# Optimization experiments

Measured on AMD Instinct MI355X. Metric: run time of the kernel, lower is better.

Reference implementation:

```python
import jax, jax.numpy as jnp
import numpy as np

B, S, D = 2, 2048, 1024
H, DK, DV = 16, 64, 64
DF = 4096
EPS = 1e-5


def _layer_norm(x, g, b):
    mu = jnp.mean(x, axis=-1, keepdims=True)
    var = jnp.mean((x - mu) ** 2, axis=-1, keepdims=True)
    return (x - mu) * jax.lax.rsqrt(var + EPS) * g + b


def setup_inputs() -> dict:
    key = jax.random.key(0)
    ks = jax.random.split(key, 12)
    s = lambda fan_in: 1.0 / np.sqrt(fan_in)
    return {
        "enc_input": jax.random.normal(ks[0], (B, S, D), dtype=jnp.float32),
        "wq": jax.random.uniform(ks[1], (D, H * DK), jnp.float32, -s(D), s(D)),
        "wk": jax.random.uniform(ks[2], (D, H * DK), jnp.float32, -s(D), s(D)),
        "wv": jax.random.uniform(ks[3], (D, H * DV), jnp.float32, -s(D), s(D)),
        "wo": jax.random.uniform(ks[4], (H * DV, D), jnp.float32, -s(H * DV), s(H * DV)),
        "w1": jax.random.uniform(ks[5], (D, DF), jnp.float32, -s(D), s(D)),
        "b1": jax.random.uniform(ks[6], (DF,), jnp.float32, -s(D), s(D)),
        "w2": jax.random.uniform(ks[7], (DF, D), jnp.float32, -s(DF), s(DF)),
        "b2": jax.random.uniform(ks[8], (D,), jnp.float32, -s(DF), s(DF)),
        "ln1_g": jnp.ones((D,), jnp.float32),
        "ln1_b": jnp.zeros((D,), jnp.float32),
        "ln2_g": jnp.ones((D,), jnp.float32),
        "ln2_b": jnp.zeros((D,), jnp.float32),
    }


def reference(enc_input, wq, wk, wv, wo, w1, b1, w2, b2, ln1_g, ln1_b, ln2_g, ln2_b):
    x = enc_input
    # QKV projections -> [B, H, S, d]
    q = (x @ wq).reshape(B, S, H, DK).transpose(0, 2, 1, 3)
    k = (x @ wk).reshape(B, S, H, DK).transpose(0, 2, 1, 3)
    v = (x @ wv).reshape(B, S, H, DV).transpose(0, 2, 1, 3)
    # scaled dot-product attention (scale = 1/sqrt(d_k), dropout is identity at eval)
    score = jnp.einsum("bhqd,bhkd->bhqk", q, k) / jnp.sqrt(jnp.float32(DK))
    attn = jax.nn.softmax(score, axis=-1)
    ctx = jnp.einsum("bhqk,bhkd->bhqd", attn, v)
    ctx = ctx.transpose(0, 2, 1, 3).reshape(B, S, H * DV)
    atn_out = ctx @ wo
    # Add & Norm 1
    h = _layer_norm(x + atn_out, ln1_g, ln1_b)
    # FFN
    ffn = jax.nn.relu(h @ w1 + b1) @ w2 + b2
    # Add & Norm 2
    return _layer_norm(h + ffn, ln2_g, ln2_b)
```

## Files before the change

kernel.cpp:

```cpp
#include <hip/hip_runtime.h>
#include <hip/hip_bf16.h>

typedef __bf16 bf16;
typedef __bf16 bf16x4 __attribute__((ext_vector_type(4)));
typedef __bf16 bf16x8 __attribute__((ext_vector_type(8)));
typedef float  f32x4  __attribute__((ext_vector_type(4)));

#define KB 2
#define KS 2048
#define KD 1024
#define KH 16
#define KM (KB*KS)
#define KQKVN 3072
#define KDF 4096

__device__ __forceinline__ f32x4 mfma16(bf16x8 a, bf16x8 b, f32x4 c) {
  return __builtin_amdgcn_mfma_f32_16x16x32_bf16(a, b, c, 0, 0, 0);
}

__device__ __forceinline__ float exp2_hw(float x) {
  float r;
  asm("v_exp_f32 %0, %1" : "=v"(r) : "v"(x));
  return r;
}

__device__ __forceinline__ void g2l16(const bf16* g, bf16* l) {
  __builtin_amdgcn_global_load_lds(
      (const __attribute__((address_space(1))) unsigned int*)g,
      (__attribute__((address_space(3))) unsigned int*)l, 16, 0, 0);
}

__global__ __launch_bounds__(256) void cvt_bf16_kernel(const float* __restrict__ in,
                                                       bf16* __restrict__ out, int n) {
  int i = (blockIdx.x * 256 + threadIdx.x) * 4;
  if (i >= n) return;
  f32x4 v = *reinterpret_cast<const f32x4*>(in + i);
  bf16x4 o;
  o[0] = (bf16)v[0]; o[1] = (bf16)v[1]; o[2] = (bf16)v[2]; o[3] = (bf16)v[3];
  *reinterpret_cast<bf16x4*>(out + i) = o;
}

struct WT4 { const float* src[4]; bf16* dst[4]; };

__global__ __launch_bounds__(256) void wtrans4_kernel(WT4 jobs) {
  __shared__ float tile[32][33];
  const float* W = jobs.src[blockIdx.z];
  bf16* WT = jobs.dst[blockIdx.z];
  const int n0 = blockIdx.x * 32, k0 = blockIdx.y * 32;
  const int tx = threadIdx.x & 31, ty = threadIdx.x >> 5;
#pragma unroll
  for (int j = ty; j < 32; j += 8) tile[j][tx] = W[(size_t)(k0 + j) * 1024 + n0 + tx];
  __syncthreads();
#pragma unroll
  for (int j = ty; j < 32; j += 8)
    WT[(size_t)(n0 + j) * 1024 + k0 + tx] = (bf16)tile[tx][j];
}

__global__ __launch_bounds__(256) void wtrans_big_kernel(const float* __restrict__ w1,
                                                         bf16* __restrict__ w1T,
                                                         const float* __restrict__ w2,
                                                         bf16* __restrict__ w2T) {
  __shared__ float tile[32][33];
  const float* W; bf16* WT; int K, N, n0, k0;
  if (blockIdx.z == 0) {
    W = w1; WT = w1T; K = 1024; N = 4096;
    n0 = blockIdx.x * 32; k0 = blockIdx.y * 32;
  } else {
    W = w2; WT = w2T; K = 4096; N = 1024;
    n0 = blockIdx.y * 32; k0 = blockIdx.x * 32;
  }
  const int tx = threadIdx.x & 31, ty = threadIdx.x >> 5;
#pragma unroll
  for (int j = ty; j < 32; j += 8) tile[j][tx] = W[(size_t)(k0 + j) * N + n0 + tx];
  __syncthreads();
#pragma unroll
  for (int j = ty; j < 32; j += 8) WT[(size_t)(n0 + j) * K + k0 + tx] = (bf16)tile[tx][j];
}

__global__ __launch_bounds__(256) void kvpack_kernel(const bf16* __restrict__ qkv,
                                                     bf16* __restrict__ kp,
                                                     bf16* __restrict__ vt) {
  __shared__ bf16 tile[64][72];
  const int s0 = blockIdx.x * 64;
  const int bh = blockIdx.y;
  const int b = bh >> 4, h = bh & 15;
  const int t = threadIdx.x;
  const int r = t >> 3, c8 = (t & 7) * 8;
#pragma unroll
  for (int rr = r; rr < 64; rr += 32) {
    const size_t grow = (size_t)(b * KS + s0 + rr) * KQKVN + h * 64 + c8;
    bf16x8 kv = *reinterpret_cast<const bf16x8*>(&qkv[grow + 1024]);
    *reinterpret_cast<bf16x8*>(&kp[((size_t)bh * KS + s0 + rr) * 64 + c8]) = kv;
    bf16x8 vv = *reinterpret_cast<const bf16x8*>(&qkv[grow + 2048]);
#pragma unroll
    for (int j = 0; j < 8; j++) tile[rr][c8 + j] = vv[j];
  }
  __syncthreads();
#pragma unroll
  for (int dd = r; dd < 64; dd += 32) {
    bf16x8 v;
#pragma unroll
    for (int j = 0; j < 8; j++) {
      const int pi = c8 + j;
      const int key = ((pi >> 5) << 5) | (((pi >> 2) & 1) << 4) |
                      (((pi >> 3) & 3) << 2) | (pi & 3);
      v[j] = tile[key][dd];
    }
    *reinterpret_cast<bf16x8*>(&vt[(size_t)bh * 64 * KS + (size_t)dd * KS + s0 + c8]) = v;
  }
}

struct P4 { bf16* p[4]; };

template <typename OUT_T, bool RELU, bool HAS_BIAS, bool SPLITK>
__global__ __launch_bounds__(512, 2) void gemm8p(const bf16* __restrict__ A,
                                                 const bf16* __restrict__ BT,
                                                 OUT_T* __restrict__ C, P4 pr,
                                                 const float* __restrict__ bias,
                                                 int M, int N, int K, int Kslice) {
  extern __shared__ __align__(16) bf16 sm[];
  const int tid = threadIdx.x, lane = tid & 63, w = tid >> 6;
  const int wr = w >> 2, wc = w & 3;
  const int gx = gridDim.x;
  const int nwg = gx * gridDim.y;
  int flat = blockIdx.y * gx + blockIdx.x;
  flat = (flat & 7) * (nwg >> 3) + (flat >> 3);
  const int bn = (flat % gx) * 256;
  const int bm = (flat / gx) * 256;
  const int z = blockIdx.z;
  const int NT = (SPLITK ? Kslice : K) >> 6;
  const int lr = lane & 15, hi = lane >> 4;
  const int sqrow = tid >> 3;
  const int sslot = tid & 7;
  const bf16* Abase = A + (size_t)bm * K + (SPLITK ? z * Kslice : 0);
  const bf16* Bbase = BT + (size_t)bn * K + (SPLITK ? z * Kslice : 0);
  auto stageQ = [&](int t, int p) {
    const int row = p * 64 + sqrow;
    const int col = (sslot ^ (row & 7)) * 8;
    bf16* dst = sm + (size_t)(t & 1) * 32768 + p * 4096 + w * 512;
    g2l16(Abase + (size_t)row * K + t * 64 + col, dst);
    g2l16(Bbase + (size_t)row * K + t * 64 + col, dst + 16384);
  };
  f32x4 acc[8][4] = {};
  stageQ(0, 0); stageQ(0, 1); stageQ(0, 2); stageQ(0, 3);
  for (int t = 0; t < NT; t++) {
    const char* sa = (const char*)(sm + (size_t)(t & 1) * 32768);
    const char* sb = sa + 32768;
    if (t + 1 < NT) {
      stageQ(t + 1, 0);
      stageQ(t + 1, 1);
      asm volatile("s_waitcnt vmcnt(4)" ::: "memory");
    } else {
      asm volatile("s_waitcnt vmcnt(0)" ::: "memory");
    }
    __builtin_amdgcn_sched_barrier(0);
    __builtin_amdgcn_s_barrier();
    __builtin_amdgcn_sched_barrier(0);
    if (t + 1 < NT) { stageQ(t + 1, 2); stageQ(t + 1, 3); }
    bf16x8 af[4], bfr[4];
#pragma unroll
    for (int mfp = 0; mfp < 4; mfp++) {
      const int row = wr * 128 + mfp * 16 + lr;
      af[mfp] = *(const bf16x8*)(sa + row * 128 + ((hi ^ (row & 7)) * 16));
    }
#pragma unroll
    for (int nf = 0; nf < 4; nf++) {
      const int row = wc * 64 + nf * 16 + lr;
      bfr[nf] = *(const bf16x8*)(sb + row * 128 + ((hi ^ (row & 7)) * 16));
    }
    __builtin_amdgcn_s_setprio(1);
#pragma unroll
    for (int mfp = 0; mfp < 4; mfp++)
#pragma unroll
      for (int nf = 0; nf < 4; nf++)
        acc[mfp][nf] = mfma16(af[mfp], bfr[nf], acc[mfp][nf]);
    __builtin_amdgcn_s_setprio(0);
#pragma unroll
    for (int mfp = 0; mfp < 4; mfp++) {
      const int row = wr * 128 + 64 + mfp * 16 + lr;
      af[mfp] = *(const bf16x8*)(sa + row * 128 + ((hi ^ (row & 7)) * 16));
    }
    __builtin_amdgcn_s_setprio(1);
#pragma unroll
    for (int mfp = 0; mfp < 4; mfp++)
#pragma unroll
      for (int nf = 0; nf < 4; nf++)
        acc[4 + mfp][nf] = mfma16(af[mfp], bfr[nf], acc[4 + mfp][nf]);
    __builtin_amdgcn_s_setprio(0);
#pragma unroll
    for (int mfp = 0; mfp < 4; mfp++) {
      const int row = wr * 128 + mfp * 16 + lr;
      af[mfp] = *(const bf16x8*)(sa + row * 128 + (((4 + hi) ^ (row & 7)) * 16));
    }
#pragma unroll
    for (int nf = 0; nf < 4; nf++) {
      const int row = wc * 64 + nf * 16 + lr;
      bfr[nf] = *(const bf16x8*)(sb + row * 128 + (((4 + hi) ^ (row & 7)) * 16));
    }
    __builtin_amdgcn_s_setprio(1);
#pragma unroll
    for (int mfp = 0; mfp < 4; mfp++)
#pragma unroll
      for (int nf = 0; nf < 4; nf++)
        acc[mfp][nf] = mfma16(af[mfp], bfr[nf], acc[mfp][nf]);
    __builtin_amdgcn_s_setprio(0);
#pragma unroll
    for (int mfp = 0; mfp < 4; mfp++) {
      const int row = wr * 128 + 64 + mfp * 16 + lr;
      af[mfp] = *(const bf16x8*)(sa + row * 128 + (((4 + hi) ^ (row & 7)) * 16));
    }
    __builtin_amdgcn_s_setprio(1);
#pragma unroll
    for (int mfp = 0; mfp < 4; mfp++)
#pragma unroll
      for (int nf = 0; nf < 4; nf++)
        acc[4 + mfp][nf] = mfma16(af[mfp], bfr[nf], acc[4 + mfp][nf]);
    __builtin_amdgcn_s_setprio(0);
    __builtin_amdgcn_sched_barrier(0);
    __builtin_amdgcn_s_barrier();
    __builtin_amdgcn_sched_barrier(0);
  }
  const int rg = hi * 4, cl = lr;
  if (SPLITK) {
    bf16* P = pr.p[z];
#pragma unroll
    for (int mf = 0; mf < 8; mf++)
#pragma unroll
      for (int nf = 0; nf < 4; nf++) {
        const int col = bn + wc * 64 + nf * 16 + cl;
#pragma unroll
        for (int i = 0; i < 4; i++) {
          const int row = bm + wr * 128 + mf * 16 + rg + i;
          P[(size_t)row * N + col] = (bf16)acc[mf][nf][i];
        }
      }
  } else {
#pragma unroll
    for (int mf = 0; mf < 8; mf++)
#pragma unroll
      for (int nf = 0; nf < 4; nf++) {
        const int col = bn + wc * 64 + nf * 16 + cl;
        float bv = 0.f;
        if (HAS_BIAS) bv = bias[col];
#pragma unroll
        for (int i = 0; i < 4; i++) {
          const int row = bm + wr * 128 + mf * 16 + rg + i;
          float v = acc[mf][nf][i] + bv;
          if (RELU) v = fmaxf(v, 0.f);
          C[(size_t)row * N + col] = (OUT_T)v;
        }
      }
  }
}

template <typename OUT_T, bool RELU, bool HAS_BIAS, int BN>
__global__ __launch_bounds__(256) void gemm_bt(const bf16* __restrict__ A,
                                               const bf16* __restrict__ BT,
                                               OUT_T* __restrict__ C,
                                               const float* __restrict__ bias,
                                               int M, int N, int K) {
  constexpr int NF = BN / 32;
  __shared__ __align__(16) bf16 sa[2][128 * 32];
  __shared__ __align__(16) bf16 sb[2][BN * 32];
  const int t = threadIdx.x, lane = t & 63, w = t >> 6;
  const int gx = gridDim.x;
  const int nwg = gx * gridDim.y;
  int flat = blockIdx.y * gx + blockIdx.x;
  if ((nwg & 7) == 0) flat = (flat & 7) * (nwg >> 3) + (flat >> 3);
  const int bn = (flat % gx) * BN;
  const int bm = (flat / gx) * 128;
  const int wr = w >> 1, wc = w & 1;
  const int wcol = wc * (BN / 2);
  const int lr = lane & 15, lk = (lane >> 4) * 8;
  const int srow = w * 16 + (lane >> 2);
  const int scol = (lane & 3) * 8;
  f32x4 acc[4][NF] = {};
  const int NT = K >> 5;
  auto stage = [&](int kt, int buf) {
#pragma unroll
    for (int i = 0; i < 2; i++)
      g2l16(A + (size_t)(bm + i * 64 + srow) * K + kt * 32 + scol,
            &sa[buf][(i * 64 + w * 16) * 32]);
#pragma unroll
    for (int i = 0; i < BN / 64; i++)
      g2l16(BT + (size_t)(bn + i * 64 + srow) * K + kt * 32 + scol,
            &sb[buf][(i * 64 + w * 16) * 32]);
  };
  stage(0, 0);
  int cur = 0;
  for (int kt = 0; kt < NT; kt++) {
    __syncthreads();
    if (kt + 1 < NT) stage(kt + 1, cur ^ 1);
    bf16x8 af[4], bfr[NF];
#pragma unroll
    for (int m = 0; m < 4; m++)
      af[m] = *(const bf16x8*)&sa[cur][(wr * 64 + m * 16 + lr) * 32 + lk];
#pragma unroll
    for (int n = 0; n < NF; n++)
      bfr[n] = *(const bf16x8*)&sb[cur][(wcol + n * 16 + lr) * 32 + lk];
#pragma unroll
    for (int m = 0; m < 4; m++)
#pragma unroll
      for (int n = 0; n < NF; n++)
        acc[m][n] = mfma16(af[m], bfr[n], acc[m][n]);
    cur ^= 1;
  }
  const int rg = (lane >> 4) * 4, cl = lane & 15;
#pragma unroll
  for (int m = 0; m < 4; m++)
#pragma unroll
    for (int n = 0; n < NF; n++) {
      const int col = bn + wcol + n * 16 + cl;
      float bv = 0.f;
      if (HAS_BIAS) bv = bias[col];
#pragma unroll
      for (int i = 0; i < 4; i++) {
        const int row = bm + wr * 64 + m * 16 + rg + i;
        float v = acc[m][n][i] + bv;
        if (RELU) v = fmaxf(v, 0.f);
        C[(size_t)row * N + col] = (OUT_T)v;
      }
    }
}

__global__ __launch_bounds__(256) void attn_kernel(const bf16* __restrict__ qkv,
                                                   const bf16* __restrict__ kp,
                                                   const bf16* __restrict__ vt,
                                                   bf16* __restrict__ ctx) {
  __shared__ __align__(16) bf16 ksm[4][64 * 64];
  __shared__ __align__(16) bf16 vsm[4][64 * 64];
  const int t = threadIdx.x, lane = t & 63, w = t >> 6;
  const int flat = blockIdx.y * 16 + blockIdx.x;
  const int xcd = flat & 7, jj = flat >> 3;
  const int bh = xcd + 8 * (jj >> 4);
  const int qb = jj & 15;
  const int b = bh >> 4, h = bh & 15;
  const int qbase = qb * 128 + w * 32;
  const int lr = lane & 15, hi = lane >> 4;
  const int lk = hi * 8, rg = hi * 4, cl = lr;

  bf16x8 aq[2][2];
#pragma unroll
  for (int m = 0; m < 2; m++)
#pragma unroll
    for (int kk = 0; kk < 2; kk++) {
      bf16x8 v = *reinterpret_cast<const bf16x8*>(
          &qkv[(size_t)(b * KS + qbase + m * 16 + lr) * KQKVN + h * 64 + kk * 32 + lk]);
#pragma unroll
      for (int e = 0; e < 8; e++) v[e] = (bf16)((float)v[e] * 0.18033688f);
      aq[m][kk] = v;
    }
  bf16x8 ones;
#pragma unroll
  for (int j = 0; j < 8; j++) ones[j] = (bf16)1.0f;

  const bf16* kpb = kp + (size_t)bh * KS * 64;
  const bf16* vtb = vt + (size_t)bh * 64 * KS;

  auto stageKV = [&](int tt) {
    const int kt0 = tt * 64;
    bf16* kd = &ksm[tt & 3][0];
    bf16* vd = &vsm[tt & 3][0];
#pragma unroll
    for (int i = 0; i < 2; i++) {
      const int q = i * 4096 + w * 1024 + (lane << 4);
      const int row = q >> 7;
      const int slot = ((q >> 4) & 7) ^ (row & 7);
      g2l16(kpb + (size_t)(kt0 + row) * 64 + slot * 8, kd + ((i * 4096 + w * 1024) >> 1));
      g2l16(vtb + (size_t)row * KS + kt0 + slot * 8,   vd + ((i * 4096 + w * 1024) >> 1));
    }
  };

  f32x4 accd[2][4] = {};
  f32x4 lsumv[2] = {};
  f32x4 sc[2][4];
#pragma unroll
  for (int m = 0; m < 2; m++)
#pragma unroll
    for (int n = 0; n < 4; n++)
#pragma unroll
      for (int e = 0; e < 4; e++) sc[m][n][e] = 0.f;

  stageKV(0); stageKV(1); stageKV(2);
  asm volatile("s_waitcnt vmcnt(8)" ::: "memory");
  __builtin_amdgcn_sched_barrier(0);
  __builtin_amdgcn_s_barrier();
  __builtin_amdgcn_sched_barrier(0);
  {
    const char* kb = (const char*)&ksm[0][0];
    bf16x8 bk[4][2];
#pragma unroll
    for (int n = 0; n < 4; n++)
#pragma unroll
      for (int kk = 0; kk < 2; kk++) {
        const int row = n * 16 + lr;
        bk[n][kk] = *(const bf16x8*)(kb + row * 128 +
                                     ((kk * 64 + hi * 16) ^ ((row & 7) << 4)));
      }
    __builtin_amdgcn_s_setprio(1);
#pragma unroll
    for (int m = 0; m < 2; m++)
#pragma unroll
      for (int n = 0; n < 4; n++)
#pragma unroll
        for (int kk = 0; kk < 2; kk++)
          sc[m][n] = mfma16(bk[n][kk], aq[m][kk], sc[m][n]);
    __builtin_amdgcn_s_setprio(0);
  }
  const int NT = KS / 64;
  for (int tt = 0; tt < NT; tt++) {
    if (tt + 1 < NT) {
      if (tt + 2 < NT) asm volatile("s_waitcnt vmcnt(4)" ::: "memory");
      else             asm volatile("s_waitcnt vmcnt(0)" ::: "memory");
      __builtin_amdgcn_sched_barrier(0);
      __builtin_amdgcn_s_barrier();
      __builtin_amdgcn_sched_barrier(0);
      if (tt + 3 < NT) stageKV(tt + 3);
    }
    bf16x8 pa[2][2];
#pragma unroll
    for (int m = 0; m < 2; m++) {
      float p[4][4];
#pragma unroll
      for (int n = 0; n < 4; n++)
#pragma unroll
        for (int i = 0; i < 4; i++)
          p[n][i] = exp2_hw(sc[m][n][i]);
#pragma unroll
      for (int kk = 0; kk < 2; kk++) {
        bf16x8 v;
#pragma unroll
        for (int j = 0; j < 8; j++) v[j] = (bf16)p[kk * 2 + (j >> 2)][j & 3];
        pa[m][kk] = v;
      }
    }
    if (tt + 1 < NT) {
      const char* kb = (const char*)&ksm[(tt + 1) & 3][0];
      bf16x8 bk[4][2];
#pragma unroll
      for (int n = 0; n < 4; n++)
#pragma unroll
        for (int kk = 0; kk < 2; kk++) {
          const int row = n * 16 + lr;
          bk[n][kk] = *(const bf16x8*)(kb + row * 128 +
                                       ((kk * 64 + hi * 16) ^ ((row & 7) << 4)));
        }
      f32x4 scn[2][4];
#pragma unroll
      for (int m = 0; m < 2; m++)
#pragma unroll
        for (int n = 0; n < 4; n++) {
#pragma unroll
          for (int e = 0; e < 4; e++) scn[m][n][e] = 0.f;
#pragma unroll
          for (int kk = 0; kk < 2; kk++)
            scn[m][n] = mfma16(bk[n][kk], aq[m][kk], scn[m][n]);
        }
#pragma unroll
      for (int m = 0; m < 2; m++)
#pragma unroll
        for (int n = 0; n < 4; n++) sc[m][n] = scn[m][n];
    }
    const char* vb = (const char*)&vsm[tt & 3][0];
    bf16x8 bv[4][2];
#pragma unroll
    for (int dt = 0; dt < 4; dt++)
#pragma unroll
      for (int kk = 0; kk < 2; kk++) {
        const int row = dt * 16 + lr;
        bv[dt][kk] = *(const bf16x8*)(vb + row * 128 +
                                      ((kk * 64 + hi * 16) ^ ((row & 7) << 4)));
      }
    __builtin_amdgcn_s_setprio(1);
#pragma unroll
    for (int m = 0; m < 2; m++) {
#pragma unroll
      for (int dt = 0; dt < 4; dt++)
#pragma unroll
        for (int kk = 0; kk < 2; kk++)
          accd[m][dt] = mfma16(pa[m][kk], bv[dt][kk], accd[m][dt]);
      lsumv[m] = mfma16(pa[m][0], ones, lsumv[m]);
      lsumv[m] = mfma16(pa[m][1], ones, lsumv[m]);
    }
    __builtin_amdgcn_s_setprio(0);
  }
#pragma unroll
  for (int m = 0; m < 2; m++)
#pragma unroll
    for (int dt = 0; dt < 4; dt++)
#pragma unroll
      for (int i = 0; i < 4; i++)
        ctx[(size_t)(b * KS + qbase + m * 16 + rg + i) * KD + h * 64 + dt * 16 + cl] =
            (bf16)(accd[m][dt][i] / lsumv[m][i]);
}

template <bool ABF, bool OBF>
__global__ __launch_bounds__(256) void ln_kernel(const void* __restrict__ aptr,
                                                 const float* __restrict__ bsum,
                                                 const float* __restrict__ g,
                                                 const float* __restrict__ bet,
                                                 void* __restrict__ outp) {
  const int row = blockIdx.x;
  const int t = threadIdx.x;
  const int lane = t & 63, wid = t >> 6;
  float v[4];
  {
    f32x4 bv = *reinterpret_cast<const f32x4*>(&bsum[(size_t)row * KD + t * 4]);
    if (ABF) {
      bf16x4 av = *reinterpret_cast<const bf16x4*>(
          (const bf16*)aptr + (size_t)row * KD + t * 4);
#pragma unroll
      for (int j = 0; j < 4; j++) v[j] = (float)av[j] + bv[j];
    } else {
      f32x4 av = *reinterpret_cast<const f32x4*>(
          (const float*)aptr + (size_t)row * KD + t * 4);
#pragma unroll
      for (int j = 0; j < 4; j++) v[j] = av[j] + bv[j];
    }
  }
  float s = 0.f, s2 = 0.f;
#pragma unroll
  for (int j = 0; j < 4; j++) { s += v[j]; s2 += v[j] * v[j]; }
#pragma unroll
  for (int off = 32; off; off >>= 1) {
    s += __shfl_xor(s, off, 64);
    s2 += __shfl_xor(s2, off, 64);
  }
  __shared__ float red[8];
  if (lane == 0) { red[wid] = s; red[wid + 4] = s2; }
  __syncthreads();
  s = red[0] + red[1] + red[2] + red[3];
  s2 = red[4] + red[5] + red[6] + red[7];
  const float mu = s * (1.f / KD);
  const float var = s2 * (1.f / KD) - mu * mu;
  const float rs = rsqrtf(var + 1e-5f);
  if (OBF) {
    bf16x4 o;
#pragma unroll
    for (int j = 0; j < 4; j++)
      o[j] = (bf16)((v[j] - mu) * rs * g[t * 4 + j] + bet[t * 4 + j]);
    *reinterpret_cast<bf16x4*>((bf16*)outp + (size_t)row * KD + t * 4) = o;
  } else {
    f32x4 o;
#pragma unroll
    for (int j = 0; j < 4; j++)
      o[j] = (v[j] - mu) * rs * g[t * 4 + j] + bet[t * 4 + j];
    *reinterpret_cast<f32x4*>((float*)outp + (size_t)row * KD + t * 4) = o;
  }
}

__global__ __launch_bounds__(256) void ln2_fused_kernel(const bf16* __restrict__ hh,
                                                        const bf16* __restrict__ p0,
                                                        const bf16* __restrict__ p1,
                                                        const bf16* __restrict__ p2,
                                                        const bf16* __restrict__ p3,
                                                        const float* __restrict__ b2,
                                                        const float* __restrict__ g,
                                                        const float* __restrict__ bet,
                                                        float* __restrict__ outp) {
  const int row = blockIdx.x;
  const int t = threadIdx.x;
  const int lane = t & 63, wid = t >> 6;
  const size_t base = (size_t)row * KD + t * 4;
  bf16x4 hv = *(const bf16x4*)(hh + base);
  bf16x4 a0 = *(const bf16x4*)(p0 + base);
  bf16x4 a1 = *(const bf16x4*)(p1 + base);
  bf16x4 a2 = *(const bf16x4*)(p2 + base);
  bf16x4 a3 = *(const bf16x4*)(p3 + base);
  f32x4 bv = *(const f32x4*)(b2 + t * 4);
  float v[4];
#pragma unroll
  for (int j = 0; j < 4; j++)
    v[j] = (float)hv[j] + (float)a0[j] + (float)a1[j] + (float)a2[j] + (float)a3[j] + bv[j];
  float s = 0.f, s2 = 0.f;
#pragma unroll
  for (int j = 0; j < 4; j++) { s += v[j]; s2 += v[j] * v[j]; }
#pragma unroll
  for (int off = 32; off; off >>= 1) {
    s += __shfl_xor(s, off, 64);
    s2 += __shfl_xor(s2, off, 64);
  }
  __shared__ float red[8];
  if (lane == 0) { red[wid] = s; red[wid + 4] = s2; }
  __syncthreads();
  s = red[0] + red[1] + red[2] + red[3];
  s2 = red[4] + red[5] + red[6] + red[7];
  const float mu = s * (1.f / KD);
  const float var = s2 * (1.f / KD) - mu * mu;
  const float rs = rsqrtf(var + 1e-5f);
  f32x4 o;
#pragma unroll
  for (int j = 0; j < 4; j++)
    o[j] = (v[j] - mu) * rs * g[t * 4 + j] + bet[t * 4 + j];
  *reinterpret_cast<f32x4*>(outp + base) = o;
}

extern "C" void kernel_launch(void* const* d_in, const int* in_sizes, int n_in,
                              void* d_out, int out_size, void* d_ws, size_t ws_size,
                              hipStream_t stream) {
  const float* x     = (const float*)d_in[0];
  const float* wq    = (const float*)d_in[1];
  const float* wk    = (const float*)d_in[2];
  const float* wv    = (const float*)d_in[3];
  const float* wo    = (const float*)d_in[4];
  const float* w1    = (const float*)d_in[5];
  const float* b1    = (const float*)d_in[6];
  const float* w2    = (const float*)d_in[7];
  const float* b2    = (const float*)d_in[8];
  const float* ln1g  = (const float*)d_in[9];
  const float* ln1b  = (const float*)d_in[10];
  const float* ln2g  = (const float*)d_in[11];
  const float* ln2b  = (const float*)d_in[12];
  float* out = (float*)d_out;

  char* ws = (char*)d_ws;
  bf16*  x_bf   = (bf16*)(ws + 0);
  bf16*  wqkvT  = (bf16*)(ws + 8388608);
  bf16*  woT    = (bf16*)(ws + 14680064);
  bf16*  w1T    = (bf16*)(ws + 16777216);
  bf16*  w2T    = (bf16*)(ws + 25165824);
  bf16*  qkv    = (bf16*)(ws + 33554432);
  bf16*  kp     = (bf16*)(ws + 58720256);
  bf16*  vt     = (bf16*)(ws + 67108864);
  float* proj   = (float*)(ws + 75497472);
  bf16*  ctx    = x_bf;
  bf16*  h_bf   = (bf16*)(ws + 8388608);
  bf16*  ffn1   = qkv;
  P4 pr;
  pr.p[0] = (bf16*)(ws + 0);
  pr.p[1] = (bf16*)(ws + 16777216);
  pr.p[2] = (bf16*)(ws + 67108864);
  pr.p[3] = (bf16*)(ws + 75497472);
  P4 pzero = {};

  cvt_bf16_kernel<<<dim3(KM * KD / 1024), 256, 0, stream>>>(x, x_bf, KM * KD);
  WT4 jobs;
  jobs.src[0] = wq; jobs.src[1] = wk; jobs.src[2] = wv; jobs.src[3] = wo;
  jobs.dst[0] = wqkvT;
  jobs.dst[1] = wqkvT + 1024 * 1024;
  jobs.dst[2] = wqkvT + 2048 * 1024;
  jobs.dst[3] = woT;
  wtrans4_kernel<<<dim3(32, 32, 4), 256, 0, stream>>>(jobs);
  wtrans_big_kernel<<<dim3(128, 32, 2), 256, 0, stream>>>(w1, w1T, w2, w2T);

  gemm8p<bf16, false, false, false>
      <<<dim3(KQKVN / 256, KM / 256, 1), 512, 131072, stream>>>(
      x_bf, wqkvT, qkv, pzero, nullptr, KM, KQKVN, KD, KD);

  kvpack_kernel<<<dim3(KS / 64, KB * KH), 256, 0, stream>>>(qkv, kp, vt);

  attn_kernel<<<dim3(KS / 128, KB * KH), 256, 0, stream>>>(qkv, kp, vt, ctx);

  gemm_bt<float, false, false, 64><<<dim3(KD / 64, KM / 128), 256, 0, stream>>>(
      ctx, woT, proj, nullptr, KM, KD, KD);

  ln_kernel<false, true><<<dim3(KM), 256, 0, stream>>>(x, proj, ln1g, ln1b, h_bf);

  gemm8p<bf16, true, true, false>
      <<<dim3(KDF / 256, KM / 256, 1), 512, 131072, stream>>>(
      h_bf, w1T, ffn1, pzero, b1, KM, KDF, KD, KD);

  gemm8p<bf16, false, false, true>
      <<<dim3(KD / 256, KM / 256, 4), 512, 131072, stream>>>(
      ffn1, w2T, (bf16*)nullptr, pr, nullptr, KM, KD, KDF, KDF / 4);

  ln2_fused_kernel<<<dim3(KM), 256, 0, stream>>>(
      h_bf, pr.p[0], pr.p[1], pr.p[2], pr.p[3], b2, ln2g, ln2b, out);
}
```

Measured before the change: 222.2 us.

## Fuse K/V repacking into QKV GEMM epilogue and use bf16 attention-projection output

The separate kvpack kernel is removed. The QKV GEMM epilogue now writes K blocks straight into per-head layout and V blocks into the transposed, permuted layout the attention kernel expects. The output projection now writes bf16 instead of fp32, and LN1 reads the bf16 x and bf16 projection, which roughly halves traffic for that step. In exchange the residual add uses bf16-rounded x and projection, which costs precision, and the K epilogue does scattered strided scalar stores.

```diff
diff --git a/kernel.cpp b/kernel.cpp
--- a/kernel.cpp
+++ b/kernel.cpp
@@ -77,42 +77,9 @@
   for (int j = ty; j < 32; j += 8) WT[(size_t)(n0 + j) * K + k0 + tx] = (bf16)tile[tx][j];
 }
 
-__global__ __launch_bounds__(256) void kvpack_kernel(const bf16* __restrict__ qkv,
-                                                     bf16* __restrict__ kp,
-                                                     bf16* __restrict__ vt) {
-  __shared__ bf16 tile[64][72];
-  const int s0 = blockIdx.x * 64;
-  const int bh = blockIdx.y;
-  const int b = bh >> 4, h = bh & 15;
-  const int t = threadIdx.x;
-  const int r = t >> 3, c8 = (t & 7) * 8;
-#pragma unroll
-  for (int rr = r; rr < 64; rr += 32) {
-    const size_t grow = (size_t)(b * KS + s0 + rr) * KQKVN + h * 64 + c8;
-    bf16x8 kv = *reinterpret_cast<const bf16x8*>(&qkv[grow + 1024]);
-    *reinterpret_cast<bf16x8*>(&kp[((size_t)bh * KS + s0 + rr) * 64 + c8]) = kv;
-    bf16x8 vv = *reinterpret_cast<const bf16x8*>(&qkv[grow + 2048]);
-#pragma unroll
-    for (int j = 0; j < 8; j++) tile[rr][c8 + j] = vv[j];
-  }
-  __syncthreads();
-#pragma unroll
-  for (int dd = r; dd < 64; dd += 32) {
-    bf16x8 v;
-#pragma unroll
-    for (int j = 0; j < 8; j++) {
-      const int pi = c8 + j;
-      const int key = ((pi >> 5) << 5) | (((pi >> 2) & 1) << 4) |
-                      (((pi >> 3) & 3) << 2) | (pi & 3);
-      v[j] = tile[key][dd];
-    }
-    *reinterpret_cast<bf16x8*>(&vt[(size_t)bh * 64 * KS + (size_t)dd * KS + s0 + c8]) = v;
-  }
-}
-
 struct P4 { bf16* p[4]; };
 
-template <typename OUT_T, bool RELU, bool HAS_BIAS, bool SPLITK>
+template <typename OUT_T, bool RELU, bool HAS_BIAS, bool SPLITK, bool QKVPACK>
 __global__ __launch_bounds__(512, 2) void gemm8p(const bf16* __restrict__ A,
                                                  const bf16* __restrict__ BT,
                                                  OUT_T* __restrict__ C, P4 pr,
@@ -221,7 +188,42 @@
     __builtin_amdgcn_sched_barrier(0);
   }
   const int rg = hi * 4, cl = lr;
-  if (SPLITK) {
+  if (QKVPACK && (bn >> 10) == 1) {
+    bf16* kp_ = pr.p[0];
+    const int b_ = bm >> 11;
+    const int sb_ = (bm & 2047) + wr * 128;
+#pragma unroll
+    for (int mf = 0; mf < 8; mf++)
+#pragma unroll
+      for (int nf = 0; nf < 4; nf++) {
+        const int col_loc = (bn & 1023) + wc * 64 + nf * 16 + cl;
+        const int hh = col_loc >> 6, dd = col_loc & 63;
+        bf16* base = kp_ + (size_t)(b_ * 16 + hh) * (KS * 64) + dd;
+#pragma unroll
+        for (int i = 0; i < 4; i++)
+          base[(size_t)(sb_ + mf * 16 + rg + i) * 64] = (bf16)acc[mf][nf][i];
+      }
+  } else if (QKVPACK && (bn >> 10) == 2) {
+    bf16* vt_ = pr.p[1];
+    const int b_ = bm >> 11;
+    const int sb_ = (bm & 2047) + wr * 128;
+    const int pib = ((hi & 2) << 3) | ((hi & 1) << 3);
+#pragma unroll
+    for (int mf = 0; mf < 8; mf++) {
+      const int s_hi = sb_ + (mf >> 2) * 64;
+      const int pibase = pib | ((mf & 2) << 4) | ((mf & 1) << 2);
+#pragma unroll
+      for (int nf = 0; nf < 4; nf++) {
+        const int col_loc = (bn & 1023) + wc * 64 + nf * 16 + cl;
+        const int hh = col_loc >> 6, dd = col_loc & 63;
+        bf16x4 o;
+#pragma unroll
+        for (int i = 0; i < 4; i++) o[i] = (bf16)acc[mf][nf][i];
+        *(bf16x4*)(vt_ + (size_t)(b_ * 16 + hh) * (64 * KS) +
+                   (size_t)dd * KS + s_hi + pibase) = o;
+      }
+    }
+  } else if (SPLITK) {
     bf16* P = pr.p[z];
 #pragma unroll
     for (int mf = 0; mf < 8; mf++)
@@ -494,9 +496,9 @@
             (bf16)(accd[m][dt][i] / lsumv[m][i]);
 }
 
-template <bool ABF, bool OBF>
+template <bool ABF, bool BBF, bool OBF>
 __global__ __launch_bounds__(256) void ln_kernel(const void* __restrict__ aptr,
-                                                 const float* __restrict__ bsum,
+                                                 const void* __restrict__ bptr,
                                                  const float* __restrict__ g,
                                                  const float* __restrict__ bet,
                                                  void* __restrict__ outp) {
@@ -505,18 +507,31 @@
   const int lane = t & 63, wid = t >> 6;
   float v[4];
   {
-    f32x4 bv = *reinterpret_cast<const f32x4*>(&bsum[(size_t)row * KD + t * 4]);
+    float a[4], bb[4];
     if (ABF) {
       bf16x4 av = *reinterpret_cast<const bf16x4*>(
           (const bf16*)aptr + (size_t)row * KD + t * 4);
 #pragma unroll
-      for (int j = 0; j < 4; j++) v[j] = (float)av[j] + bv[j];
+      for (int j = 0; j < 4; j++) a[j] = (float)av[j];
     } else {
       f32x4 av = *reinterpret_cast<const f32x4*>(
           (const float*)aptr + (size_t)row * KD + t * 4);
 #pragma unroll
-      for (int j = 0; j < 4; j++) v[j] = av[j] + bv[j];
-    }
+      for (int j = 0; j < 4; j++) a[j] = av[j];
+    }
+    if (BBF) {
+      bf16x4 bv = *reinterpret_cast<const bf16x4*>(
+          (const bf16*)bptr + (size_t)row * KD + t * 4);
+#pragma unroll
+      for (int j = 0; j < 4; j++) bb[j] = (float)bv[j];
+    } else {
+      f32x4 bv = *reinterpret_cast<const f32x4*>(
+          (const float*)bptr + (size_t)row * KD + t * 4);
+#pragma unroll
+      for (int j = 0; j < 4; j++) bb[j] = bv[j];
+    }
+#pragma unroll
+    for (int j = 0; j < 4; j++) v[j] = a[j] + bb[j];
   }
   float s = 0.f, s2 = 0.f;
 #pragma unroll
@@ -622,10 +637,12 @@
   bf16*  qkv    = (bf16*)(ws + 33554432);
   bf16*  kp     = (bf16*)(ws + 58720256);
   bf16*  vt     = (bf16*)(ws + 67108864);
-  float* proj   = (float*)(ws + 75497472);
-  bf16*  ctx    = x_bf;
+  bf16*  ctx    = (bf16*)(ws + 75497472);
+  bf16*  proj_bf= (bf16*)(ws + 83886080);
   bf16*  h_bf   = (bf16*)(ws + 8388608);
   bf16*  ffn1   = qkv;
+  P4 pk;
+  pk.p[0] = kp; pk.p[1] = vt; pk.p[2] = nullptr; pk.p[3] = nullptr;
   P4 pr;
   pr.p[0] = (bf16*)(ws + 0);
   pr.p[1] = (bf16*)(ws + 16777216);
@@ -643,24 +660,23 @@
   wtrans4_kernel<<<dim3(32, 32, 4), 256, 0, stream>>>(jobs);
   wtrans_big_kernel<<<dim3(128, 32, 2), 256, 0, stream>>>(w1, w1T, w2, w2T);
 
-  gemm8p<bf16, false, false, false>
+  gemm8p<bf16, false, false, false, true>
       <<<dim3(KQKVN / 256, KM / 256, 1), 512, 131072, stream>>>(
-      x_bf, wqkvT, qkv, pzero, nullptr, KM, KQKVN, KD, KD);
-
-  kvpack_kernel<<<dim3(KS / 64, KB * KH), 256, 0, stream>>>(qkv, kp, vt);
+      x_bf, wqkvT, qkv, pk, nullptr, KM, KQKVN, KD, KD);
 
   attn_kernel<<<dim3(KS / 128, KB * KH), 256, 0, stream>>>(qkv, kp, vt, ctx);
 
-  gemm_bt<float, false, false, 64><<<dim3(KD / 64, KM / 128), 256, 0, stream>>>(
-      ctx, woT, proj, nullptr, KM, KD, KD);
-
-  ln_kernel<false, true><<<dim3(KM), 256, 0, stream>>>(x, proj, ln1g, ln1b, h_bf);
-
-  gemm8p<bf16, true, true, false>
+  gemm_bt<bf16, false, false, 64><<<dim3(KD / 64, KM / 128), 256, 0, stream>>>(
+      ctx, woT, proj_bf, nullptr, KM, KD, KD);
+
+  ln_kernel<true, true, true><<<dim3(KM), 256, 0, stream>>>(
+      x_bf, proj_bf, ln1g, ln1b, h_bf);
+
+  gemm8p<bf16, true, true, false, false>
       <<<dim3(KDF / 256, KM / 256, 1), 512, 131072, stream>>>(
       h_bf, w1T, ffn1, pzero, b1, KM, KDF, KD, KD);
 
-  gemm8p<bf16, false, false, true>
+  gemm8p<bf16, false, false, true, false>
       <<<dim3(KD / 256, KM / 256, 4), 512, 131072, stream>>>(
       ffn1, w2T, (bf16*)nullptr, pr, nullptr, KM, KD, KDF, KDF / 4);
 
```

Measured after the change: 214.7 us, median of 2. 1.04x faster.
